# Kernel optimization log

Measured on AMD Instinct MI355X. Metric: run time of the kernel, lower is better.

The kernel has to match this reference:

```python
import jax, jax.numpy as jnp
import numpy as np

D = 2048      # input_dim
E = 16        # num_experts
H = 1024      # expert_units
K = 4         # k_top
B = 4096      # batch


def setup_inputs() -> dict:
    key = jax.random.key(0)
    ks = jax.random.split(key, 7)
    s1 = 1.0 / np.sqrt(D)
    s2 = 1.0 / np.sqrt(H)
    return {
        "x": jax.random.normal(ks[0], (B, D), dtype=jnp.float32),
        "W1": jax.random.uniform(ks[1], (E, D, H), jnp.float32, -s1, s1),
        "b1": jax.random.uniform(ks[2], (E, H), jnp.float32, -s1, s1),
        "W2": jax.random.uniform(ks[3], (E, H, D), jnp.float32, -s2, s2),
        "b2": jax.random.uniform(ks[4], (E, D), jnp.float32, -s2, s2),
        "Wr": jax.random.uniform(ks[5], (D, E), jnp.float32, -s1, s1),
        "br": jax.random.uniform(ks[6], (E,), jnp.float32, -s1, s1),
    }


def reference(x, W1, b1, W2, b2, Wr, br):
    # Router + top-k (torch.topk returns sorted descending; lax.top_k matches)
    logits = x @ Wr + br                          # [B, E]
    top_w, top_i = jax.lax.top_k(logits, K)       # [B, K]
    top_w = jax.nn.softmax(top_w, axis=1)

    # Dense all-expert MLP (eval mode: dropout is identity)
    h = jax.nn.relu(jnp.einsum('bd,edh->beh', x, W1) + b1)   # [B, E, H]
    expert_out = jnp.einsum('beh,ehd->bed', h, W2) + b2      # [B, E, D]

    # mask/detach trick: forward value is unchanged (identity in fwd)
    mask = jax.nn.one_hot(top_i, E, dtype=expert_out.dtype).sum(axis=1)  # [B, E]
    m = mask[:, :, None]
    expert_out = expert_out * m + jax.lax.stop_gradient(expert_out * (1.0 - m))

    # Gather top-k experts and combine
    sel = jnp.take_along_axis(expert_out, top_i[:, :, None], axis=1)    # [B, K, D]
    out = (sel * top_w[:, :, None]).sum(axis=1)
    return out + x
```

## Files before the change

### kernel.cpp

```cpp
#include <hip/hip_runtime.h>
#include <math.h>

#define D_   2048
#define E_   16
#define H_   1024
#define KSEL 4
#define B_   4096
#define CAP  4096

typedef short bf16x8_t __attribute__((ext_vector_type(8)));
typedef float f32x4_t  __attribute__((ext_vector_type(4)));

__device__ __forceinline__ unsigned short f2bf(float f) {
  unsigned u = __float_as_uint(f);
  u += 0x7FFFu + ((u >> 16) & 1u);
  return (unsigned short)(u >> 16);
}

__device__ __forceinline__ float bf2f(unsigned short h) {
  unsigned u = (unsigned)h << 16;
  return __uint_as_float(u);
}

__device__ __forceinline__ void gld16(const void* g, void* l) {
  __builtin_amdgcn_global_load_lds(
      (const __attribute__((address_space(1))) unsigned int*)g,
      (__attribute__((address_space(3))) unsigned int*)l, 16, 0, 0);
}

__global__ void k_prep(const float* __restrict__ x, unsigned short* __restrict__ xb) {
  int i = blockIdx.x * 256 + threadIdx.x;
  float4 v = ((const float4*)x)[i];
  ushort4 o;
  o.x = f2bf(v.x); o.y = f2bf(v.y); o.z = f2bf(v.z); o.w = f2bf(v.w);
  ((ushort4*)xb)[i] = o;
}

__global__ void k_transw(const float* __restrict__ in, unsigned short* __restrict__ out,
                         int R, int C) {
  __shared__ float tile[32][33];
  size_t ebase = (size_t)blockIdx.z * R * C;
  in += ebase; out += ebase;
  int c0 = blockIdx.x * 32, r0 = blockIdx.y * 32;
  int tx = threadIdx.x;
#pragma unroll
  for (int i = threadIdx.y; i < 32; i += 8)
    tile[i][tx] = in[(size_t)(r0 + i) * C + c0 + tx];
  __syncthreads();
#pragma unroll
  for (int i = threadIdx.y; i < 32; i += 8)
    out[(size_t)(c0 + i) * R + r0 + tx] = f2bf(tile[tx][i]);
}

__global__ void k_transr(const float* __restrict__ in, float* __restrict__ out) {
  int i = blockIdx.x * 256 + threadIdx.x;
  int d = i >> 4, e = i & 15;
  out[e * D_ + d] = in[i];
}

__global__ __launch_bounds__(256) void k_router(
    const float* __restrict__ x, const float* __restrict__ wrT, const float* __restrict__ br,
    int* __restrict__ tops, float* __restrict__ topw) {
  int wid = threadIdx.x >> 6, lane = threadIdx.x & 63;
  int t = blockIdx.x * 4 + wid;
  float acc[E_];
#pragma unroll
  for (int e = 0; e < E_; e++) acc[e] = 0.f;
  const float4* xr = (const float4*)(x + (size_t)t * D_);
#pragma unroll
  for (int j = 0; j < D_ / 256; j++) {
    float4 xv = xr[j * 64 + lane];
#pragma unroll
    for (int e = 0; e < E_; e++) {
      float4 wv = ((const float4*)(wrT + (size_t)e * D_))[j * 64 + lane];
      acc[e] += xv.x * wv.x + xv.y * wv.y + xv.z * wv.z + xv.w * wv.w;
    }
  }
#pragma unroll
  for (int e = 0; e < E_; e++) {
    float v = acc[e];
    for (int m = 32; m >= 1; m >>= 1) v += __shfl_xor(v, m);
    acc[e] = v;
  }
  if (lane == 0) {
    float lg[E_];
#pragma unroll
    for (int e = 0; e < E_; e++) lg[e] = acc[e] + br[e];
    unsigned used = 0; int sel[KSEL]; float sv[KSEL];
    for (int k = 0; k < KSEL; k++) {
      float best = -1e30f; int bi = 0;
      for (int e = 0; e < E_; e++)
        if (!((used >> e) & 1u) && lg[e] > best) { best = lg[e]; bi = e; }
      used |= 1u << bi; sel[k] = bi; sv[k] = best;
    }
    float mx = sv[0], s = 0.f, w[KSEL];
    for (int k = 0; k < KSEL; k++) { w[k] = expf(sv[k] - mx); s += w[k]; }
    float inv = 1.f / s;
    int4 ti; float4 tw;
    ti.x = sel[0]; ti.y = sel[1]; ti.z = sel[2]; ti.w = sel[3];
    tw.x = w[0] * inv; tw.y = w[1] * inv; tw.z = w[2] * inv; tw.w = w[3] * inv;
    ((int4*)tops)[t] = ti;
    ((float4*)topw)[t] = tw;
  }
}

__global__ __launch_bounds__(256) void k_build(
    const int* __restrict__ tops, const float* __restrict__ topw,
    int* __restrict__ counts, int* __restrict__ ids, float* __restrict__ wts,
    int* __restrict__ inv) {
  int e = blockIdx.x;
  int tid = threadIdx.x, lane = tid & 63, wid = tid >> 6;
  __shared__ int wsum[4];
  __shared__ int red[4];
  int base = 0;
  int pre = 0;
  for (int c = 0; c < B_; c += 256) {
    int t = c + tid;
    int4 tk = ((const int4*)tops)[t];
    pre += (tk.x < e) + (tk.y < e) + (tk.z < e) + (tk.w < e);
    int k = -1;
    if (tk.x == e) k = 0; else if (tk.y == e) k = 1;
    else if (tk.z == e) k = 2; else if (tk.w == e) k = 3;
    unsigned long long mask = __ballot(k >= 0);
    int myoff = __popcll(mask & ((1ull << lane) - 1ull));
    if (lane == 0) wsum[wid] = __popcll(mask);
    __syncthreads();
    int woff = 0;
#pragma unroll
    for (int i = 0; i < 4; i++) if (i < wid) woff += wsum[i];
    int ctotal = wsum[0] + wsum[1] + wsum[2] + wsum[3];
    if (k >= 0) {
      int slot = base + woff + myoff;
      ids[e * CAP + slot] = t;
      wts[e * CAP + slot] = topw[t * 4 + k];
    }
    base += ctotal;
    __syncthreads();
  }
  if (tid == 0) counts[e] = base;
  for (int m = 32; m >= 1; m >>= 1) pre += __shfl_xor(pre, m);
  if (lane == 0) red[wid] = pre;
  __syncthreads();
  int offe = red[0] + red[1] + red[2] + red[3];
  for (int s = tid; s < base; s += 256) {
    int t = ids[e * CAP + s];
    int4 tk = ((const int4*)tops)[t];
    int k = (tk.x == e) ? 0 : (tk.y == e) ? 1 : (tk.z == e) ? 2 : 3;
    inv[t * 4 + k] = offe + s;
  }
}

__global__ __launch_bounds__(256) void k_gather(
    const float* __restrict__ x, const unsigned short* __restrict__ ybuf,
    const int* __restrict__ inv, float* __restrict__ out) {
  int t = blockIdx.x;
  int4 iv = ((const int4*)inv)[t];
  const ushort4* y0 = (const ushort4*)(ybuf + (size_t)iv.x * D_);
  const ushort4* y1 = (const ushort4*)(ybuf + (size_t)iv.y * D_);
  const ushort4* y2 = (const ushort4*)(ybuf + (size_t)iv.z * D_);
  const ushort4* y3 = (const ushort4*)(ybuf + (size_t)iv.w * D_);
  const float4* xr = (const float4*)(x + (size_t)t * D_);
  float4* orow = (float4*)(out + (size_t)t * D_);
#pragma unroll
  for (int i = threadIdx.x; i < D_ / 4; i += 256) {
    float4 v = xr[i];
    ushort4 a = y0[i], b = y1[i], c = y2[i], d = y3[i];
    v.x += bf2f(a.x) + bf2f(b.x) + bf2f(c.x) + bf2f(d.x);
    v.y += bf2f(a.y) + bf2f(b.y) + bf2f(c.y) + bf2f(d.y);
    v.z += bf2f(a.z) + bf2f(b.z) + bf2f(c.z) + bf2f(d.z);
    v.w += bf2f(a.w) + bf2f(b.w) + bf2f(c.w) + bf2f(d.w);
    orow[i] = v;
  }
}


__global__ __launch_bounds__(256, 2) void k_gemm1(
    const unsigned short* __restrict__ xb,
    const unsigned short* __restrict__ w1t,
    const float* __restrict__ b1,
    const int* __restrict__ ids, const int* __restrict__ counts,
    unsigned short* __restrict__ hbuf)
{
  __shared__ unsigned short As[128 * 64];
  __shared__ unsigned short Bs[256 * 64];
  int cnts[E_], offsv[E_], rowt[E_];
  int s = 0, ntr = 0;
#pragma unroll
  for (int e = 0; e < E_; e++) {
    cnts[e] = counts[e];
    offsv[e] = s; s += cnts[e];
    rowt[e] = (cnts[e] + 127) >> 7; ntr += rowt[e];
  }
  const int NS = H_ / 256;
  int totalTiles = ntr * NS;
  int tid = threadIdx.x, lane = tid & 63, wid = tid >> 6;
  int wr = wid >> 1, wc = wid & 1;
  int cr = lane >> 3, slot = lane & 7;
  int sw = (slot ^ cr) << 3;
  int hi = lane >> 4, cl = lane & 15;
  int bswz = (blockIdx.x & 7) * (gridDim.x >> 3) + (blockIdx.x >> 3);

  for (int tile = bswz; tile < totalTiles; tile += gridDim.x) {
    int slab = tile / ntr;
    int rtg = tile - slab * ntr;
    int n0 = slab << 8;
    int e = 0, base = 0;
    while (e < E_ - 1 && rtg >= base + rowt[e]) { base += rowt[e]; e++; }
    int rt = rtg - base;
    int cnt = cnts[e];
    int r0 = rt << 7;

    const unsigned short* a_src[4];
    const unsigned short* b_src[8];
    const unsigned short* wbase = w1t + (size_t)e * H_ * D_;
#pragma unroll
    for (int i = 0; i < 4; i++) {
      int chunk = wid * 4 + i;
      int rr = r0 + chunk * 8 + cr;
      int rc = min(rr, cnt - 1);
      int tok = ids[e * CAP + rc];
      a_src[i] = xb + (size_t)tok * D_ + sw;
    }
#pragma unroll
    for (int i = 0; i < 8; i++) {
      int chunk = wid * 8 + i;
      b_src[i] = wbase + (size_t)(n0 + chunk * 8 + cr) * D_ + sw;
    }
    f32x4_t acc[4][8];
#pragma unroll
    for (int m = 0; m < 4; m++)
#pragma unroll
      for (int n = 0; n < 8; n++) acc[m][n] = (f32x4_t){0.f, 0.f, 0.f, 0.f};

    for (int kt = 0; kt < D_; kt += 64) {
#pragma unroll
      for (int i = 0; i < 4; i++)
        gld16(a_src[i] + kt, As + (wid * 4 + i) * 512);
#pragma unroll
      for (int i = 0; i < 8; i++)
        gld16(b_src[i] + kt, Bs + (wid * 8 + i) * 512);
      __syncthreads();
#pragma unroll
      for (int kb = 0; kb < 2; kb++) {
        bf16x8_t af[4], bfr[8];
#pragma unroll
        for (int m = 0; m < 4; m++) {
          int row = wr * 64 + m * 16 + (lane & 15);
          int ss = (kb * 4 + (lane >> 4)) ^ (row & 7);
          af[m] = *(const bf16x8_t*)(As + row * 64 + ss * 8);
        }
#pragma unroll
        for (int n = 0; n < 8; n++) {
          int row = wc * 128 + n * 16 + (lane & 15);
          int ss = (kb * 4 + (lane >> 4)) ^ (row & 7);
          bfr[n] = *(const bf16x8_t*)(Bs + row * 64 + ss * 8);
        }
#pragma unroll
        for (int m = 0; m < 4; m++)
#pragma unroll
          for (int n = 0; n < 8; n++)
            acc[m][n] = __builtin_amdgcn_mfma_f32_16x16x32_bf16(af[m], bfr[n], acc[m][n], 0, 0, 0);
      }
      __syncthreads();
    }
    int offe = offsv[e];
    float bias[8];
#pragma unroll
    for (int n = 0; n < 8; n++)
      bias[n] = b1[e * H_ + n0 + wc * 128 + n * 16 + cl];
#pragma unroll
    for (int m = 0; m < 4; m++)
#pragma unroll
      for (int j = 0; j < 4; j++) {
        int sr = r0 + wr * 64 + m * 16 + hi * 4 + j;
        if (sr < cnt) {
          size_t rowb = (size_t)(offe + sr) * H_;
#pragma unroll
          for (int n = 0; n < 8; n++) {
            int col = n0 + wc * 128 + n * 16 + cl;
            float v = acc[m][n][j] + bias[n];
            v = v > 0.f ? v : 0.f;
            hbuf[rowb + col] = f2bf(v);
          }
        }
      }
  }
}

__global__ __launch_bounds__(256, 2) void k_gemm2(
    const unsigned short* __restrict__ hbuf,
    const unsigned short* __restrict__ w2t,
    const float* __restrict__ b2,
    const float* __restrict__ wts,
    const int* __restrict__ counts,
    unsigned short* __restrict__ ybuf)
{
  __shared__ unsigned short As[128 * 64];
  __shared__ unsigned short Bs[256 * 64];
  int cnts[E_], offsv[E_], rowt[E_];
  int s = 0, ntr = 0;
#pragma unroll
  for (int e = 0; e < E_; e++) {
    cnts[e] = counts[e];
    offsv[e] = s; s += cnts[e];
    rowt[e] = (cnts[e] + 127) >> 7; ntr += rowt[e];
  }
  const int NS = D_ / 256;
  int totalTiles = ntr * NS;
  int tid = threadIdx.x, lane = tid & 63, wid = tid >> 6;
  int wr = wid >> 1, wc = wid & 1;
  int cr = lane >> 3, slot = lane & 7;
  int sw = (slot ^ cr) << 3;
  int hi = lane >> 4, cl = lane & 15;
  int bswz = (blockIdx.x & 7) * (gridDim.x >> 3) + (blockIdx.x >> 3);

  for (int tile = bswz; tile < totalTiles; tile += gridDim.x) {
    int slab = tile / ntr;
    int rtg = tile - slab * ntr;
    int n0 = slab << 8;
    int e = 0, base = 0;
    while (e < E_ - 1 && rtg >= base + rowt[e]) { base += rowt[e]; e++; }
    int rt = rtg - base;
    int cnt = cnts[e];
    int r0 = rt << 7;
    int offe = offsv[e];

    const unsigned short* a_src[4];
    const unsigned short* b_src[8];
    const unsigned short* wbase = w2t + (size_t)e * D_ * H_;
#pragma unroll
    for (int i = 0; i < 4; i++) {
      int chunk = wid * 4 + i;
      int rr = r0 + chunk * 8 + cr;
      int rc = min(rr, cnt - 1);
      a_src[i] = hbuf + (size_t)(offe + rc) * H_ + sw;
    }
#pragma unroll
    for (int i = 0; i < 8; i++) {
      int chunk = wid * 8 + i;
      b_src[i] = wbase + (size_t)(n0 + chunk * 8 + cr) * H_ + sw;
    }
    f32x4_t acc[4][8];
#pragma unroll
    for (int m = 0; m < 4; m++)
#pragma unroll
      for (int n = 0; n < 8; n++) acc[m][n] = (f32x4_t){0.f, 0.f, 0.f, 0.f};

    for (int kt = 0; kt < H_; kt += 64) {
#pragma unroll
      for (int i = 0; i < 4; i++)
        gld16(a_src[i] + kt, As + (wid * 4 + i) * 512);
#pragma unroll
      for (int i = 0; i < 8; i++)
        gld16(b_src[i] + kt, Bs + (wid * 8 + i) * 512);
      __syncthreads();
#pragma unroll
      for (int kb = 0; kb < 2; kb++) {
        bf16x8_t af[4], bfr[8];
#pragma unroll
        for (int m = 0; m < 4; m++) {
          int row = wr * 64 + m * 16 + (lane & 15);
          int ss = (kb * 4 + (lane >> 4)) ^ (row & 7);
          af[m] = *(const bf16x8_t*)(As + row * 64 + ss * 8);
        }
#pragma unroll
        for (int n = 0; n < 8; n++) {
          int row = wc * 128 + n * 16 + (lane & 15);
          int ss = (kb * 4 + (lane >> 4)) ^ (row & 7);
          bfr[n] = *(const bf16x8_t*)(Bs + row * 64 + ss * 8);
        }
#pragma unroll
        for (int m = 0; m < 4; m++)
#pragma unroll
          for (int n = 0; n < 8; n++)
            acc[m][n] = __builtin_amdgcn_mfma_f32_16x16x32_bf16(af[m], bfr[n], acc[m][n], 0, 0, 0);
      }
      __syncthreads();
    }
    float bias[8];
#pragma unroll
    for (int n = 0; n < 8; n++)
      bias[n] = b2[e * D_ + n0 + wc * 128 + n * 16 + cl];
#pragma unroll
    for (int m = 0; m < 4; m++)
#pragma unroll
      for (int j = 0; j < 4; j++) {
        int sr = r0 + wr * 64 + m * 16 + hi * 4 + j;
        if (sr < cnt) {
          float w = wts[e * CAP + sr];
          unsigned short* yrow = ybuf + (size_t)(offe + sr) * D_;
#pragma unroll
          for (int n = 0; n < 8; n++) {
            int col = n0 + wc * 128 + n * 16 + cl;
            yrow[col] = f2bf(w * (acc[m][n][j] + bias[n]));
          }
        }
      }
  }
}

extern "C" void kernel_launch(void* const* d_in, const int* in_sizes, int n_in,
                              void* d_out, int out_size, void* d_ws, size_t ws_size,
                              hipStream_t stream) {
  const float* x  = (const float*)d_in[0];
  const float* W1 = (const float*)d_in[1];
  const float* b1 = (const float*)d_in[2];
  const float* W2 = (const float*)d_in[3];
  const float* b2 = (const float*)d_in[4];
  const float* Wr = (const float*)d_in[5];
  const float* br = (const float*)d_in[6];
  float* out = (float*)d_out;
  char* ws = (char*)d_ws;
  unsigned short* W1t  = (unsigned short*)(ws);
  unsigned short* ybuf = (unsigned short*)(ws);
  unsigned short* W2t  = (unsigned short*)(ws + 67108864);
  unsigned short* xb   = (unsigned short*)(ws + 134217728);
  unsigned short* hb   = (unsigned short*)(ws + 150994944);
  int*   ids    = (int*)  (ws + 184549376);
  float* wts    = (float*)(ws + 184811520);
  int*   counts = (int*)  (ws + 185073664);
  float* wrT    = (float*)(ws + 185073728);
  int*   tops   = (int*)  (ws + 185204800);
  float* topw   = (float*)(ws + 185270336);
  int*   inv    = (int*)  (ws + 185335872);

  k_prep<<<8192, 256, 0, stream>>>(x, xb);
  k_transr<<<128, 256, 0, stream>>>(Wr, wrT);
  k_transw<<<dim3(32, 64, 16), dim3(32, 8), 0, stream>>>(W1, W1t, 2048, 1024);
  k_transw<<<dim3(64, 32, 16), dim3(32, 8), 0, stream>>>(W2, W2t, 1024, 2048);
  k_router<<<1024, 256, 0, stream>>>(x, wrT, br, tops, topw);
  k_build<<<16, 256, 0, stream>>>(tops, topw, counts, ids, wts, inv);
  k_gemm1<<<512, 256, 0, stream>>>(xb, W1t, b1, ids, counts, hb);
  k_gemm2<<<1024, 256, 0, stream>>>(hb, W2t, b2, wts, counts, ybuf);
  k_gather<<<4096, 256, 0, stream>>>(x, ybuf, inv, out);
}
```

Baseline: 479.6 us.

## Triple-buffer grouped GEMM LDS pipeline with 8 waves and counted waits

Both grouped expert GEMMs move from a single-buffered load/sync/compute loop to a 3-stage LDS ring. Tiles for k+2 are issued asynchronously while tile k is computed, and barriers wait on partial vmcnt. Blocks grow to 512 threads with a 2x4 wave layout (each wave 64x64), use setprio around the MFMA sections, and launch with fewer persistent blocks. The weight transpose also writes packed ushort2 pairs. The point is to hide global-to-LDS latency behind MFMA work, at the cost of triple the LDS per block (144 KB), which limits occupancy.

```diff
diff --git a/kernel.cpp b/kernel.cpp
--- a/kernel.cpp
+++ b/kernel.cpp
@@ -42,14 +42,19 @@
   size_t ebase = (size_t)blockIdx.z * R * C;
   in += ebase; out += ebase;
   int c0 = blockIdx.x * 32, r0 = blockIdx.y * 32;
-  int tx = threadIdx.x;
-#pragma unroll
-  for (int i = threadIdx.y; i < 32; i += 8)
+  int tx = threadIdx.x & 31, ty = threadIdx.x >> 5;
+#pragma unroll
+  for (int i = ty; i < 32; i += 8)
     tile[i][tx] = in[(size_t)(r0 + i) * C + c0 + tx];
   __syncthreads();
 #pragma unroll
-  for (int i = threadIdx.y; i < 32; i += 8)
-    out[(size_t)(c0 + i) * R + r0 + tx] = f2bf(tile[tx][i]);
+  for (int w = threadIdx.x; w < 32 * 16; w += 256) {
+    int i = w >> 4, rp = w & 15;
+    ushort2 v;
+    v.x = f2bf(tile[2 * rp][i]);
+    v.y = f2bf(tile[2 * rp + 1][i]);
+    *(ushort2*)(out + (size_t)(c0 + i) * R + r0 + 2 * rp) = v;
+  }
 }
 
 __global__ void k_transr(const float* __restrict__ in, float* __restrict__ out) {
@@ -173,16 +178,61 @@
   }
 }
 
-
-__global__ __launch_bounds__(256, 2) void k_gemm1(
+#define GSTAGE(ASb, BSb, ktt) do {                                   \
+    int ko_ = (ktt) * 64;                                            \
+    _Pragma("unroll")                                                \
+    for (int i_ = 0; i_ < 2; i_++)                                   \
+      gld16(a_src[i_] + ko_, (ASb) + (wid * 2 + i_) * 512);          \
+    _Pragma("unroll")                                                \
+    for (int j_ = 0; j_ < 4; j_++)                                   \
+      gld16(b_src[j_] + ko_, (BSb) + (wid * 4 + j_) * 512);          \
+  } while (0)
+
+#define GCOMPUTE(ASb, BSb) do {                                      \
+    __builtin_amdgcn_s_setprio(1);                                   \
+    _Pragma("unroll")                                                \
+    for (int kb = 0; kb < 2; kb++) {                                 \
+      bf16x8_t af[4], bfr[4];                                        \
+      _Pragma("unroll")                                              \
+      for (int m = 0; m < 4; m++) {                                  \
+        int row = wm * 64 + m * 16 + (lane & 15);                    \
+        int ss = (kb * 4 + (lane >> 4)) ^ (row & 7);                 \
+        af[m] = *(const bf16x8_t*)((ASb) + row * 64 + ss * 8);       \
+      }                                                              \
+      _Pragma("unroll")                                              \
+      for (int n = 0; n < 4; n++) {                                  \
+        int row = wn * 64 + n * 16 + (lane & 15);                    \
+        int ss = (kb * 4 + (lane >> 4)) ^ (row & 7);                 \
+        bfr[n] = *(const bf16x8_t*)((BSb) + row * 64 + ss * 8);      \
+      }                                                              \
+      _Pragma("unroll")                                              \
+      for (int m = 0; m < 4; m++)                                    \
+        _Pragma("unroll")                                            \
+        for (int n = 0; n < 4; n++)                                  \
+          acc[m][n] = __builtin_amdgcn_mfma_f32_16x16x32_bf16(       \
+              af[m], bfr[n], acc[m][n], 0, 0, 0);                    \
+    }                                                                \
+    __builtin_amdgcn_s_setprio(0);                                   \
+  } while (0)
+
+#define GBAR_COUNTED(cond) do {                                      \
+    if (cond) asm volatile("s_waitcnt vmcnt(6)" ::: "memory");       \
+    else      asm volatile("s_waitcnt vmcnt(0)" ::: "memory");       \
+    __builtin_amdgcn_sched_barrier(0);                               \
+    __builtin_amdgcn_s_barrier();                                    \
+    __builtin_amdgcn_sched_barrier(0);                               \
+  } while (0)
+
+__global__ __launch_bounds__(512, 2) void k_gemm1(
     const unsigned short* __restrict__ xb,
     const unsigned short* __restrict__ w1t,
     const float* __restrict__ b1,
     const int* __restrict__ ids, const int* __restrict__ counts,
     unsigned short* __restrict__ hbuf)
 {
-  __shared__ unsigned short As[128 * 64];
-  __shared__ unsigned short Bs[256 * 64];
+  __shared__ unsigned short As[3][128 * 64];
+  __shared__ unsigned short Bs[3][256 * 64];
+  const int NKT = D_ / 64;
   int cnts[E_], offsv[E_], rowt[E_];
   int s = 0, ntr = 0;
 #pragma unroll
@@ -194,7 +244,7 @@
   const int NS = H_ / 256;
   int totalTiles = ntr * NS;
   int tid = threadIdx.x, lane = tid & 63, wid = tid >> 6;
-  int wr = wid >> 1, wc = wid & 1;
+  int wm = wid >> 2, wn = wid & 3;
   int cr = lane >> 3, slot = lane & 7;
   int sw = (slot ^ cr) << 3;
   int hi = lane >> 4, cl = lane & 15;
@@ -210,74 +260,58 @@
     int cnt = cnts[e];
     int r0 = rt << 7;
 
-    const unsigned short* a_src[4];
-    const unsigned short* b_src[8];
+    const unsigned short* a_src[2];
+    const unsigned short* b_src[4];
     const unsigned short* wbase = w1t + (size_t)e * H_ * D_;
 #pragma unroll
-    for (int i = 0; i < 4; i++) {
-      int chunk = wid * 4 + i;
+    for (int i = 0; i < 2; i++) {
+      int chunk = wid * 2 + i;
       int rr = r0 + chunk * 8 + cr;
       int rc = min(rr, cnt - 1);
       int tok = ids[e * CAP + rc];
       a_src[i] = xb + (size_t)tok * D_ + sw;
     }
 #pragma unroll
-    for (int i = 0; i < 8; i++) {
-      int chunk = wid * 8 + i;
-      b_src[i] = wbase + (size_t)(n0 + chunk * 8 + cr) * D_ + sw;
-    }
-    f32x4_t acc[4][8];
+    for (int j = 0; j < 4; j++) {
+      int chunk = wid * 4 + j;
+      b_src[j] = wbase + (size_t)(n0 + chunk * 8 + cr) * D_ + sw;
+    }
+    f32x4_t acc[4][4];
 #pragma unroll
     for (int m = 0; m < 4; m++)
 #pragma unroll
-      for (int n = 0; n < 8; n++) acc[m][n] = (f32x4_t){0.f, 0.f, 0.f, 0.f};
-
-    for (int kt = 0; kt < D_; kt += 64) {
-#pragma unroll
-      for (int i = 0; i < 4; i++)
-        gld16(a_src[i] + kt, As + (wid * 4 + i) * 512);
-#pragma unroll
-      for (int i = 0; i < 8; i++)
-        gld16(b_src[i] + kt, Bs + (wid * 8 + i) * 512);
-      __syncthreads();
-#pragma unroll
-      for (int kb = 0; kb < 2; kb++) {
-        bf16x8_t af[4], bfr[8];
-#pragma unroll
-        for (int m = 0; m < 4; m++) {
-          int row = wr * 64 + m * 16 + (lane & 15);
-          int ss = (kb * 4 + (lane >> 4)) ^ (row & 7);
-          af[m] = *(const bf16x8_t*)(As + row * 64 + ss * 8);
-        }
-#pragma unroll
-        for (int n = 0; n < 8; n++) {
-          int row = wc * 128 + n * 16 + (lane & 15);
-          int ss = (kb * 4 + (lane >> 4)) ^ (row & 7);
-          bfr[n] = *(const bf16x8_t*)(Bs + row * 64 + ss * 8);
-        }
-#pragma unroll
-        for (int m = 0; m < 4; m++)
-#pragma unroll
-          for (int n = 0; n < 8; n++)
-            acc[m][n] = __builtin_amdgcn_mfma_f32_16x16x32_bf16(af[m], bfr[n], acc[m][n], 0, 0, 0);
+      for (int n = 0; n < 4; n++) acc[m][n] = (f32x4_t){0.f, 0.f, 0.f, 0.f};
+
+    GSTAGE(As[0], Bs[0], 0);
+    GSTAGE(As[1], Bs[1], 1);
+    asm volatile("s_waitcnt vmcnt(6)" ::: "memory");
+    __builtin_amdgcn_sched_barrier(0);
+    __builtin_amdgcn_s_barrier();
+    __builtin_amdgcn_sched_barrier(0);
+    for (int kt = 0; kt < NKT; kt++) {
+      int cur = kt % 3;
+      if (kt + 2 < NKT) {
+        int nb = (kt + 2) % 3;
+        GSTAGE(As[nb], Bs[nb], kt + 2);
       }
-      __syncthreads();
+      GCOMPUTE(As[cur], Bs[cur]);
+      GBAR_COUNTED(kt + 2 < NKT);
     }
     int offe = offsv[e];
-    float bias[8];
-#pragma unroll
-    for (int n = 0; n < 8; n++)
-      bias[n] = b1[e * H_ + n0 + wc * 128 + n * 16 + cl];
+    float bias[4];
+#pragma unroll
+    for (int n = 0; n < 4; n++)
+      bias[n] = b1[e * H_ + n0 + wn * 64 + n * 16 + cl];
 #pragma unroll
     for (int m = 0; m < 4; m++)
 #pragma unroll
       for (int j = 0; j < 4; j++) {
-        int sr = r0 + wr * 64 + m * 16 + hi * 4 + j;
+        int sr = r0 + wm * 64 + m * 16 + hi * 4 + j;
         if (sr < cnt) {
           size_t rowb = (size_t)(offe + sr) * H_;
 #pragma unroll
-          for (int n = 0; n < 8; n++) {
-            int col = n0 + wc * 128 + n * 16 + cl;
+          for (int n = 0; n < 4; n++) {
+            int col = n0 + wn * 64 + n * 16 + cl;
             float v = acc[m][n][j] + bias[n];
             v = v > 0.f ? v : 0.f;
             hbuf[rowb + col] = f2bf(v);
@@ -287,7 +321,7 @@
   }
 }
 
-__global__ __launch_bounds__(256, 2) void k_gemm2(
+__global__ __launch_bounds__(512, 2) void k_gemm2(
     const unsigned short* __restrict__ hbuf,
     const unsigned short* __restrict__ w2t,
     const float* __restrict__ b2,
@@ -295,8 +329,9 @@
     const int* __restrict__ counts,
     unsigned short* __restrict__ ybuf)
 {
-  __shared__ unsigned short As[128 * 64];
-  __shared__ unsigned short Bs[256 * 64];
+  __shared__ unsigned short As[3][128 * 64];
+  __shared__ unsigned short Bs[3][256 * 64];
+  const int NKT = H_ / 64;
   int cnts[E_], offsv[E_], rowt[E_];
   int s = 0, ntr = 0;
 #pragma unroll
@@ -308,7 +343,7 @@
   const int NS = D_ / 256;
   int totalTiles = ntr * NS;
   int tid = threadIdx.x, lane = tid & 63, wid = tid >> 6;
-  int wr = wid >> 1, wc = wid & 1;
+  int wm = wid >> 2, wn = wid & 3;
   int cr = lane >> 3, slot = lane & 7;
   int sw = (slot ^ cr) << 3;
   int hi = lane >> 4, cl = lane & 15;
@@ -325,73 +360,57 @@
     int r0 = rt << 7;
     int offe = offsv[e];
 
-    const unsigned short* a_src[4];
-    const unsigned short* b_src[8];
+    const unsigned short* a_src[2];
+    const unsigned short* b_src[4];
     const unsigned short* wbase = w2t + (size_t)e * D_ * H_;
 #pragma unroll
-    for (int i = 0; i < 4; i++) {
-      int chunk = wid * 4 + i;
+    for (int i = 0; i < 2; i++) {
+      int chunk = wid * 2 + i;
       int rr = r0 + chunk * 8 + cr;
       int rc = min(rr, cnt - 1);
       a_src[i] = hbuf + (size_t)(offe + rc) * H_ + sw;
     }
 #pragma unroll
-    for (int i = 0; i < 8; i++) {
-      int chunk = wid * 8 + i;
-      b_src[i] = wbase + (size_t)(n0 + chunk * 8 + cr) * H_ + sw;
-    }
-    f32x4_t acc[4][8];
+    for (int j = 0; j < 4; j++) {
+      int chunk = wid * 4 + j;
+      b_src[j] = wbase + (size_t)(n0 + chunk * 8 + cr) * H_ + sw;
+    }
+    f32x4_t acc[4][4];
 #pragma unroll
     for (int m = 0; m < 4; m++)
 #pragma unroll
-      for (int n = 0; n < 8; n++) acc[m][n] = (f32x4_t){0.f, 0.f, 0.f, 0.f};
-
-    for (int kt = 0; kt < H_; kt += 64) {
-#pragma unroll
-      for (int i = 0; i < 4; i++)
-        gld16(a_src[i] + kt, As + (wid * 4 + i) * 512);
-#pragma unroll
-      for (int i = 0; i < 8; i++)
-        gld16(b_src[i] + kt, Bs + (wid * 8 + i) * 512);
-      __syncthreads();
-#pragma unroll
-      for (int kb = 0; kb < 2; kb++) {
-        bf16x8_t af[4], bfr[8];
-#pragma unroll
-        for (int m = 0; m < 4; m++) {
-          int row = wr * 64 + m * 16 + (lane & 15);
-          int ss = (kb * 4 + (lane >> 4)) ^ (row & 7);
-          af[m] = *(const bf16x8_t*)(As + row * 64 + ss * 8);
-        }
-#pragma unroll
-        for (int n = 0; n < 8; n++) {
-          int row = wc * 128 + n * 16 + (lane & 15);
-          int ss = (kb * 4 + (lane >> 4)) ^ (row & 7);
-          bfr[n] = *(const bf16x8_t*)(Bs + row * 64 + ss * 8);
-        }
-#pragma unroll
-        for (int m = 0; m < 4; m++)
-#pragma unroll
-          for (int n = 0; n < 8; n++)
-            acc[m][n] = __builtin_amdgcn_mfma_f32_16x16x32_bf16(af[m], bfr[n], acc[m][n], 0, 0, 0);
+      for (int n = 0; n < 4; n++) acc[m][n] = (f32x4_t){0.f, 0.f, 0.f, 0.f};
+
+    GSTAGE(As[0], Bs[0], 0);
+    GSTAGE(As[1], Bs[1], 1);
+    asm volatile("s_waitcnt vmcnt(6)" ::: "memory");
+    __builtin_amdgcn_sched_barrier(0);
+    __builtin_amdgcn_s_barrier();
+    __builtin_amdgcn_sched_barrier(0);
+    for (int kt = 0; kt < NKT; kt++) {
+      int cur = kt % 3;
+      if (kt + 2 < NKT) {
+        int nb = (kt + 2) % 3;
+        GSTAGE(As[nb], Bs[nb], kt + 2);
       }
-      __syncthreads();
-    }
-    float bias[8];
-#pragma unroll
-    for (int n = 0; n < 8; n++)
-      bias[n] = b2[e * D_ + n0 + wc * 128 + n * 16 + cl];
+      GCOMPUTE(As[cur], Bs[cur]);
+      GBAR_COUNTED(kt + 2 < NKT);
+    }
+    float bias[4];
+#pragma unroll
+    for (int n = 0; n < 4; n++)
+      bias[n] = b2[e * D_ + n0 + wn * 64 + n * 16 + cl];
 #pragma unroll
     for (int m = 0; m < 4; m++)
 #pragma unroll
       for (int j = 0; j < 4; j++) {
-        int sr = r0 + wr * 64 + m * 16 + hi * 4 + j;
+        int sr = r0 + wm * 64 + m * 16 + hi * 4 + j;
         if (sr < cnt) {
           float w = wts[e * CAP + sr];
           unsigned short* yrow = ybuf + (size_t)(offe + sr) * D_;
 #pragma unroll
-          for (int n = 0; n < 8; n++) {
-            int col = n0 + wc * 128 + n * 16 + cl;
+          for (int n = 0; n < 4; n++) {
+            int col = n0 + wn * 64 + n * 16 + cl;
             yrow[col] = f2bf(w * (acc[m][n][j] + bias[n]));
           }
         }
@@ -426,11 +445,11 @@
 
   k_prep<<<8192, 256, 0, stream>>>(x, xb);
   k_transr<<<128, 256, 0, stream>>>(Wr, wrT);
-  k_transw<<<dim3(32, 64, 16), dim3(32, 8), 0, stream>>>(W1, W1t, 2048, 1024);
-  k_transw<<<dim3(64, 32, 16), dim3(32, 8), 0, stream>>>(W2, W2t, 1024, 2048);
+  k_transw<<<dim3(32, 64, 16), 256, 0, stream>>>(W1, W1t, 2048, 1024);
+  k_transw<<<dim3(64, 32, 16), 256, 0, stream>>>(W2, W2t, 1024, 2048);
   k_router<<<1024, 256, 0, stream>>>(x, wrT, br, tops, topw);
   k_build<<<16, 256, 0, stream>>>(tops, topw, counts, ids, wts, inv);
-  k_gemm1<<<512, 256, 0, stream>>>(xb, W1t, b1, ids, counts, hb);
-  k_gemm2<<<1024, 256, 0, stream>>>(hb, W2t, b2, wts, counts, ybuf);
+  k_gemm1<<<256, 512, 0, stream>>>(xb, W1t, b1, ids, counts, hb);
+  k_gemm2<<<256, 512, 0, stream>>>(hb, W2t, b2, wts, counts, ybuf);
   k_gather<<<4096, 256, 0, stream>>>(x, ybuf, inv, out);
 }
```

Result: slower. 518.8 us (+8.2%).
